# Kernel optimization log

Hardware: AMD Instinct MI355X
Metric: run time of the kernel (lower is better)

## Reference

```python
import jax, jax.numpy as jnp
import numpy as np

B, L, H = 64, 512, 512  # batch_size, input_size (src len), hidden_size


def setup_inputs() -> dict:
    key = jax.random.key(0)
    ks = jax.random.split(key, 12)
    return {
        "encoder_outputs": jax.random.normal(ks[0], (B, L, H), dtype=jnp.float32),
        "attn_mask": jax.random.randint(ks[1], (B, L), 0, 2, dtype=jnp.int64),
        "hidden": jax.random.normal(ks[2], (B, H), dtype=jnp.float32),
        "coverage": jax.random.uniform(ks[3], (B, L), dtype=jnp.float32),
        # attnLin: Linear(H, H)
        "attn_w": jax.random.normal(ks[4], (H, H), dtype=jnp.float32) * 0.02,
        "attn_b": jax.random.normal(ks[5], (H,), dtype=jnp.float32) * 0.02,
        # decoderAttnLinear: Linear(H, H)
        "dec_w": jax.random.normal(ks[6], (H, H), dtype=jnp.float32) * 0.02,
        "dec_b": jax.random.normal(ks[7], (H,), dtype=jnp.float32) * 0.02,
        # cvgConv: Conv2d(L, L, kernel=(1, H), padding='same') -> weight [L, L, 1, H]
        "cvg_w": jax.random.normal(ks[8], (L, L, 1, H), dtype=jnp.float32) * 0.02,
        "cvg_b": jax.random.normal(ks[9], (L,), dtype=jnp.float32) * 0.02,
        # v parameter (trunc_normal in torch; plain normal is fine as a baseline)
        "v": jax.random.normal(ks[10], (B, H), dtype=jnp.float32),
    }


def reference(encoder_outputs, attn_mask, hidden, coverage,
              attn_w, attn_b, dec_w, dec_b, cvg_w, cvg_b, v):
    # Per-position linear loop in torch == one batched linear over [B, L, H].
    enc_feat = jnp.einsum('blh,oh->blo', encoder_outputs, attn_w) + attn_b  # [B,L,H]
    dec_feat = (hidden @ dec_w.T + dec_b)[:, None, :]                        # [B,1,H]
    # Coverage conv: input is [B, L(channels), 1, 1]; kernel (1, H) with 'same'
    # padding means only kernel column kw = (H-1)//2 ever overlaps the single
    # real (non-zero-padded) pixel, so the conv reduces exactly to a matmul
    # with that weight column plus bias. Same math, no wasted zero-multiplies.
    center = (H - 1) // 2
    w_eff = cvg_w[:, :, 0, center]                                           # [L_out, L_in]
    cov_feat = (coverage @ w_eff.T + cvg_b)[:, :, None]                      # [B,L,1]
    feats = jnp.tanh(enc_feat + dec_feat + cov_feat)                         # [B,L,H]
    scores = jnp.einsum('blh,bh->bl', feats, v)                              # [B,L]
    scores = jnp.where(attn_mask == 1, scores, -jnp.inf)
    attn_weights = jax.nn.softmax(scores, axis=1)                            # [B,L]
    new_coverage = coverage + attn_weights                                   # coverage += aw
    context_vector = jnp.einsum('bl,blh->bh', attn_weights, encoder_outputs) # [B,H]
    return context_vector, attn_weights, new_coverage
```

## Files before the change

kernel.cpp:

```cpp
#include <hip/hip_runtime.h>

#define B_ 64
#define L_ 512
#define H_ 512
#define CENTER 255

typedef float  f32x4  __attribute__((ext_vector_type(4)));
typedef _Float16 f16x8 __attribute__((ext_vector_type(8)));
typedef unsigned short u16x4 __attribute__((ext_vector_type(4)));
typedef unsigned short u16x8 __attribute__((ext_vector_type(8)));
typedef unsigned short USH;


__device__ __forceinline__ float fast_tanh(float x) {
    float e = __expf(2.0f * x);
    return 1.0f - 2.0f * __builtin_amdgcn_rcpf(e + 1.0f);
}

__launch_bounds__(512)
__global__ void pre_kernel(const float* __restrict__ cvg_w, const float* __restrict__ cvg_b,
                           const float* __restrict__ coverage,
                           const float* __restrict__ aw, USH* __restrict__ bh16,
                           const float* __restrict__ hidden, const float* __restrict__ dec_w,
                           const float* __restrict__ dec_b,
                           float* __restrict__ dec_feat, float* __restrict__ cov_feat) {
    __shared__ float pool[34304];
    const int bid = blockIdx.x, t = threadIdx.x;
    if (bid < 512) {
        float* wl = pool;
        float* cs = pool + 512;
        const int i = bid;
        wl[t] = cvg_w[((size_t)(i * L_ + t)) * H_ + CENTER];
        #pragma unroll 8
        for (int c = 0; c < 64; ++c)
            cs[t * 65 + c] = coverage[c * L_ + t];
        __syncthreads();
        const int b = t >> 3, jg = t & 7;
        float sum = 0.f;
        #pragma unroll 8
        for (int jj = 0; jj < 64; ++jj) {
            int j = jg * 64 + ((jj + jg * 8) & 63);
            sum += cs[j * 65 + b] * wl[j];
        }
        sum += __shfl_xor(sum, 1, 64);
        sum += __shfl_xor(sum, 2, 64);
        sum += __shfl_xor(sum, 4, 64);
        if (jg == 0) cov_feat[b * L_ + i] = sum + cvg_b[i];
    } else if (bid < 640) {
        int i = (bid - 512) * 512 + t;
        float4 x = *(const float4*)&aw[(size_t)i * 4];
        float xs[4] = {x.x, x.y, x.z, x.w};
        u16x4 h;
        #pragma unroll
        for (int j = 0; j < 4; ++j)
            h[j] = __builtin_bit_cast(USH, (_Float16)xs[j]);
        *(u16x4*)&bh16[(size_t)i * 4] = h;
    } else {
        float* sbuf = pool;
        float* pr   = pool + 512;
        const int blk = bid - 640, b = blk >> 2, qq = blk & 3;
        const int ol = t & 127, part = t >> 7;
        sbuf[t] = hidden[b * H_ + t];
        __syncthreads();
        const float* row  = dec_w + (size_t)(qq * 128 + ol) * H_ + part * 128;
        const float* hseg = sbuf + part * 128;
        float d0 = 0.f, d1 = 0.f, d2 = 0.f, d3 = 0.f;
        #pragma unroll
        for (int k = 0; k < 128; k += 16) {
            float4 w0 = *(const float4*)&row[k];
            float4 w1 = *(const float4*)&row[k + 4];
            float4 w2 = *(const float4*)&row[k + 8];
            float4 w3 = *(const float4*)&row[k + 12];
            d0 += w0.x * hseg[k]      + w0.y * hseg[k + 1]  + w0.z * hseg[k + 2]  + w0.w * hseg[k + 3];
            d1 += w1.x * hseg[k + 4]  + w1.y * hseg[k + 5]  + w1.z * hseg[k + 6]  + w1.w * hseg[k + 7];
            d2 += w2.x * hseg[k + 8]  + w2.y * hseg[k + 9]  + w2.z * hseg[k + 10] + w2.w * hseg[k + 11];
            d3 += w3.x * hseg[k + 12] + w3.y * hseg[k + 13] + w3.z * hseg[k + 14] + w3.w * hseg[k + 15];
        }
        pr[t] = d0 + d1 + d2 + d3;
        __syncthreads();
        if (t < 128)
            dec_feat[b * H_ + qq * 128 + t] = pr[t] + pr[t + 128] + pr[t + 256] + pr[t + 384]
                                              + dec_b[qq * 128 + t];
    }
}

#define BM 128

#define STAGE_B(BUF, KS1)                                                                  \
    {                                                                                      \
        _Pragma("unroll")                                                                  \
        for (int it = 0; it < 2; ++it)                                                     \
            __builtin_amdgcn_global_load_lds(                                              \
                (const __attribute__((address_space(1))) void*)(bh16 + goffB[it] + (KS1) * 32), \
                (__attribute__((address_space(3))) void*)&Bsh[BUF][(wv * 2 + it) * 512],   \
                16, 0, 0);                                                                 \
    }

#define CVTWRITEA2(BUF, A4a, A4b)                                                          \
    {                                                                                      \
        float axs[8] = {A4a.x, A4a.y, A4a.z, A4a.w, A4b.x, A4b.y, A4b.z, A4b.w};           \
        u16x8 hh;                                                                          \
        _Pragma("unroll")                                                                  \
        for (int j = 0; j < 8; ++j)                                                        \
            hh[j] = __builtin_bit_cast(USH, (_Float16)axs[j]);                             \
        *(u16x8*)&Ash[BUF][awoff] = hh;                                                    \
    }

__launch_bounds__(512, 4)
__global__ void fused_score_mfma(const float* __restrict__ enc,
                                 const USH* __restrict__ bh16,
                                 const float* __restrict__ attn_b,
                                 const float* __restrict__ dec_feat,
                                 const float* __restrict__ cov_feat,
                                 const float* __restrict__ v,
                                 float* __restrict__ spart) {
    __shared__ USH Bsh[3][8192];
    __shared__ USH Ash[2][4096];

    const int t  = threadIdx.x;
    const int wv = t >> 6, ln = t & 63;
    const int wr = wv >> 2, wc = wv & 3;
    const int q  = ln >> 4, cl = ln & 15;
    const int mt = blockIdx.x, half = blockIdx.y;
    const int m0 = mt * BM;
    const int b  = mt >> 2;
    const int n0 = half * 256;

    int goffB[2];
    #pragma unroll
    for (int it = 0; it < 2; ++it) {
        int c   = wv * 2 + it;
        int srl = ln >> 3;
        int u   = (ln & 7) ^ (srl & 7);
        int n   = n0 + c * 16 + srl * 2 + (u >> 2);
        goffB[it] = n * 512 + (u & 3) * 8;
    }
    const int sA   = (((cl & 1) * 4 + q) ^ ((cl >> 1) & 7)) * 8;
    const int aoff = wr * 2048 + (cl >> 1) * 64 + sA;
    const int boff = wc * 2048 + (cl >> 1) * 64 + sA;

    const int arow = t >> 2, ak4 = t & 3;
    const int asw  = ((arow & 1) * 4 + ak4) ^ ((arow >> 1) & 7);
    const int awoff = (arow >> 1) * 64 + asw * 8;
    const float* agsrc = enc + (size_t)(m0 + arow) * H_ + ak4 * 8;

    f32x4 acc[4][4];
    #pragma unroll
    for (int mf = 0; mf < 4; ++mf)
        #pragma unroll
        for (int nf = 0; nf < 4; ++nf) acc[mf][nf] = (f32x4){0.f, 0.f, 0.f, 0.f};

    float4 aPa = *(const float4*)(agsrc + 32);
    float4 aPb = *(const float4*)(agsrc + 36);
    float4 c0a = *(const float4*)agsrc;
    float4 c0b = *(const float4*)(agsrc + 4);
    __builtin_amdgcn_sched_barrier(0);
    STAGE_B(0, 0);
    STAGE_B(1, 1);
    __builtin_amdgcn_sched_barrier(0);
    CVTWRITEA2(0, c0a, c0b);
    asm volatile("s_waitcnt lgkmcnt(0)" ::: "memory");
    asm volatile("s_waitcnt vmcnt(2)" ::: "memory");
    __builtin_amdgcn_sched_barrier(0);
    __builtin_amdgcn_s_barrier();

    #pragma unroll
    for (int ks = 0; ks < 16; ++ks) {
        const int curB = ks % 3;
        const int curA = ks & 1, nxtA = curA ^ 1;
        float4 aNa, aNb;
        if (ks < 14) {
            STAGE_B((ks + 2) % 3, ks + 2);
            aNa = *(const float4*)(agsrc + (ks + 2) * 32);
            aNb = *(const float4*)(agsrc + (ks + 2) * 32 + 4);
            __builtin_amdgcn_sched_barrier(0);
        }

        f16x8 ah[4];
        #pragma unroll
        for (int mf = 0; mf < 4; ++mf)
            ah[mf] = *(const f16x8*)&Ash[curA][aoff + mf * 512];
        __builtin_amdgcn_s_setprio(1);
        #pragma unroll
        for (int nf = 0; nf < 4; ++nf) {
            f16x8 bh = *(const f16x8*)&Bsh[curB][boff + nf * 512];
            #pragma unroll
            for (int mf = 0; mf < 4; ++mf)
                acc[mf][nf] = __builtin_amdgcn_mfma_f32_16x16x32_f16(ah[mf], bh, acc[mf][nf], 0, 0, 0);
        }
        __builtin_amdgcn_s_setprio(0);

        if (ks < 15) {
            CVTWRITEA2(nxtA, aPa, aPb);
            aPa = aNa; aPb = aNb;
            asm volatile("s_waitcnt lgkmcnt(0)" ::: "memory");
            if (ks < 14)
                asm volatile("s_waitcnt vmcnt(4)" ::: "memory");
            else
                asm volatile("s_waitcnt vmcnt(0)" ::: "memory");
            __builtin_amdgcn_sched_barrier(0);
            __builtin_amdgcn_s_barrier();
        }
    }
    __syncthreads();

    float (*scred)[BM] = (float (*)[BM])Ash;
    float addv[4], vvv[4];
    #pragma unroll
    for (int nf = 0; nf < 4; ++nf) {
        int n = n0 + wc * 64 + nf * 16 + cl;
        addv[nf] = attn_b[n] + dec_feat[b * H_ + n];
        vvv[nf]  = v[b * H_ + n];
    }
    #pragma unroll
    for (int mf = 0; mf < 4; ++mf) {
        #pragma unroll
        for (int reg = 0; reg < 4; ++reg) {
            int row = wr * 64 + mf * 16 + q * 4 + reg;
            float cf = cov_feat[m0 + row];
            float s = 0.f;
            #pragma unroll
            for (int nf = 0; nf < 4; ++nf)
                s += fast_tanh(acc[mf][nf][reg] + addv[nf] + cf) * vvv[nf];
            s += __shfl_xor(s, 1, 64);
            s += __shfl_xor(s, 2, 64);
            s += __shfl_xor(s, 4, 64);
            s += __shfl_xor(s, 8, 64);
            if (cl == 0) scred[wc][row] = s;
        }
    }
    __syncthreads();
    if (t < BM) {
        float s = 0.f;
        #pragma unroll
        for (int g = 0; g < 4; ++g) s += scred[g][t];
        spart[half * (B_ * L_) + m0 + t] = s;
    }
}

__launch_bounds__(1024)
__global__ void smctx_kernel(const float* __restrict__ spart, const int* __restrict__ mask,
                             const float* __restrict__ coverage, const float* __restrict__ enc,
                             float* __restrict__ out) {
    __shared__ float w[512];
    __shared__ float red[16];
    __shared__ float red2[16];
    __shared__ float4 cred4[32][32];
    const int bid = blockIdx.x, b = bid >> 2, hc = bid & 3, t = threadIdx.x;
    const int wv = t >> 6, ln = t & 63;

    float sv = 0.f; bool mk = false;
    if (t < 512) {
        mk = (mask[b * L_ + t] == 1);
        sv = spart[b * L_ + t] + spart[B_ * L_ + b * L_ + t];
    }
    float val = (t < 512 && mk) ? sv : -INFINITY;

    float r = val;
    #pragma unroll
    for (int d = 1; d <= 32; d <<= 1) r = fmaxf(r, __shfl_xor(r, d, 64));
    if (ln == 0) red[wv] = r;
    __syncthreads();
    float gmax = red[0];
    #pragma unroll
    for (int i = 1; i < 16; ++i) gmax = fmaxf(gmax, red[i]);

    float p = (t < 512 && mk) ? __expf(sv - gmax) : 0.f;
    float qq = p;
    #pragma unroll
    for (int d = 1; d <= 32; d <<= 1) qq += __shfl_xor(qq, d, 64);
    if (ln == 0) red2[wv] = qq;
    __syncthreads();
    float tot = 0.f;
    #pragma unroll
    for (int i = 0; i < 16; ++i) tot += red2[i];

    float wt = p / tot;
    if (t < 512) {
        w[t] = wt;
        if (hc == 0) {
            out[B_ * H_ + b * L_ + t] = wt;
            out[B_ * H_ + B_ * L_ + b * L_ + t] = coverage[b * L_ + t] + wt;
        }
    }
    __syncthreads();

    const int c4 = t & 31, rg = t >> 5;
    const float4* ebase = (const float4*)enc
                          + ((size_t)(b * L_ + rg)) * 128 + hc * 32 + c4;
    float4 a4 = {0.f, 0.f, 0.f, 0.f};
    #pragma unroll
    for (int k = 0; k < 16; ++k) {
        float wl_ = w[rg + 32 * k];
        float4 e = ebase[(size_t)(32 * k) * 128];
        a4.x += wl_ * e.x; a4.y += wl_ * e.y; a4.z += wl_ * e.z; a4.w += wl_ * e.w;
    }
    cred4[rg][c4] = a4;
    __syncthreads();
    if (t < 32) {
        float4 s = {0.f, 0.f, 0.f, 0.f};
        #pragma unroll
        for (int g = 0; g < 32; ++g) {
            float4 c = cred4[g][t];
            s.x += c.x; s.y += c.y; s.z += c.z; s.w += c.w;
        }
        *(float4*)&out[b * H_ + hc * 128 + t * 4] = s;
    }
}

extern "C" void kernel_launch(void* const* d_in, const int* in_sizes, int n_in,
                              void* d_out, int out_size, void* d_ws, size_t ws_size,
                              hipStream_t stream) {
    const float* enc      = (const float*)d_in[0];
    const int*   mask     = (const int*)d_in[1];
    const float* hidden   = (const float*)d_in[2];
    const float* coverage = (const float*)d_in[3];
    const float* attn_w   = (const float*)d_in[4];
    const float* attn_b   = (const float*)d_in[5];
    const float* dec_w    = (const float*)d_in[6];
    const float* dec_b    = (const float*)d_in[7];
    const float* cvg_w    = (const float*)d_in[8];
    const float* cvg_b    = (const float*)d_in[9];
    const float* v        = (const float*)d_in[10];
    float* out = (float*)d_out;
    float* ws  = (float*)d_ws;
    float* dec_feat = ws + 32768;
    float* cov_feat = ws + 65536;
    float* spart    = ws + 98304;
    USH* bpk = (USH*)(ws + 360448);

    hipLaunchKernelGGL(pre_kernel,       dim3(896),     dim3(512),  0, stream,
                       cvg_w, cvg_b, coverage, attn_w, bpk, hidden, dec_w, dec_b,
                       dec_feat, cov_feat);
    hipLaunchKernelGGL(fused_score_mfma, dim3(256, 2),  dim3(512),  0, stream,
                       enc, bpk, attn_b, dec_feat, cov_feat, v, spart);
    hipLaunchKernelGGL(smctx_kernel,     dim3(256),     dim3(1024), 0, stream,
                       spart, mask, coverage, enc, out);
}
```

Baseline: 67.43 us.

## Merge pre_kernel's three block roles into uniform 256-block launch

Replaces the heterogeneous 896-block pre_kernel (separate blocks for coverage conv, weight fp16 conversion, and decoder linear) with 256 uniform blocks that each do all three jobs: two coverage-conv outputs, a slice of the weight conversion, and a quarter-row of the decoder linear. The coverage tile load is shared across two output columns and the wave-count imbalance between block types is removed. In exchange, each block uses more LDS (about 136 KB for the full cs array plus buffers), which limits occupancy, and the kernel runs fewer, longer blocks.

```diff
diff --git a/kernel.cpp b/kernel.cpp
--- a/kernel.cpp
+++ b/kernel.cpp
@@ -24,30 +24,18 @@
                            const float* __restrict__ hidden, const float* __restrict__ dec_w,
                            const float* __restrict__ dec_b,
                            float* __restrict__ dec_feat, float* __restrict__ cov_feat) {
-    __shared__ float pool[34304];
+    __shared__ float wl2[1024];
+    __shared__ float cs[512 * 65];
+    __shared__ float sbuf[512];
+    __shared__ float pr[512];
     const int bid = blockIdx.x, t = threadIdx.x;
-    if (bid < 512) {
-        float* wl = pool;
-        float* cs = pool + 512;
-        const int i = bid;
-        wl[t] = cvg_w[((size_t)(i * L_ + t)) * H_ + CENTER];
-        #pragma unroll 8
-        for (int c = 0; c < 64; ++c)
-            cs[t * 65 + c] = coverage[c * L_ + t];
-        __syncthreads();
-        const int b = t >> 3, jg = t & 7;
-        float sum = 0.f;
-        #pragma unroll 8
-        for (int jj = 0; jj < 64; ++jj) {
-            int j = jg * 64 + ((jj + jg * 8) & 63);
-            sum += cs[j * 65 + b] * wl[j];
-        }
-        sum += __shfl_xor(sum, 1, 64);
-        sum += __shfl_xor(sum, 2, 64);
-        sum += __shfl_xor(sum, 4, 64);
-        if (jg == 0) cov_feat[b * L_ + i] = sum + cvg_b[i];
-    } else if (bid < 640) {
-        int i = (bid - 512) * 512 + t;
+    const int i0 = bid, i1 = bid + 256;
+
+    wl2[t]       = cvg_w[((size_t)(i0 * L_ + t)) * H_ + CENTER];
+    wl2[512 + t] = cvg_w[((size_t)(i1 * L_ + t)) * H_ + CENTER];
+
+    if (t < 256) {
+        int i = bid * 256 + t;
         float4 x = *(const float4*)&aw[(size_t)i * 4];
         float xs[4] = {x.x, x.y, x.z, x.w};
         u16x4 h;
@@ -55,13 +43,14 @@
         for (int j = 0; j < 4; ++j)
             h[j] = __builtin_bit_cast(USH, (_Float16)xs[j]);
         *(u16x4*)&bh16[(size_t)i * 4] = h;
-    } else {
-        float* sbuf = pool;
-        float* pr   = pool + 512;
-        const int blk = bid - 640, b = blk >> 2, qq = blk & 3;
-        const int ol = t & 127, part = t >> 7;
-        sbuf[t] = hidden[b * H_ + t];
-        __syncthreads();
+    }
+
+    const int b = bid >> 2, qq = bid & 3;
+    const int ol = t & 127, part = t >> 7;
+    sbuf[t] = hidden[b * H_ + t];
+    __syncthreads();
+
+    {
         const float* row  = dec_w + (size_t)(qq * 128 + ol) * H_ + part * 128;
         const float* hseg = sbuf + part * 128;
         float d0 = 0.f, d1 = 0.f, d2 = 0.f, d3 = 0.f;
@@ -77,10 +66,37 @@
             d3 += w3.x * hseg[k + 12] + w3.y * hseg[k + 13] + w3.z * hseg[k + 14] + w3.w * hseg[k + 15];
         }
         pr[t] = d0 + d1 + d2 + d3;
-        __syncthreads();
-        if (t < 128)
-            dec_feat[b * H_ + qq * 128 + t] = pr[t] + pr[t + 128] + pr[t + 256] + pr[t + 384]
-                                              + dec_b[qq * 128 + t];
+    }
+
+    #pragma unroll 8
+    for (int c = 0; c < 64; ++c)
+        cs[t * 65 + c] = coverage[c * L_ + t];
+    __syncthreads();
+
+    if (t < 128)
+        dec_feat[b * H_ + qq * 128 + t] = pr[t] + pr[t + 128] + pr[t + 256] + pr[t + 384]
+                                          + dec_b[qq * 128 + t];
+
+    {
+        const int bb = t >> 3, jg = t & 7;
+        float s0 = 0.f, s1 = 0.f;
+        #pragma unroll 8
+        for (int jj = 0; jj < 64; ++jj) {
+            int j = jg * 64 + ((jj + jg * 8) & 63);
+            float c = cs[j * 65 + bb];
+            s0 += c * wl2[j];
+            s1 += c * wl2[512 + j];
+        }
+        s0 += __shfl_xor(s0, 1, 64);
+        s0 += __shfl_xor(s0, 2, 64);
+        s0 += __shfl_xor(s0, 4, 64);
+        s1 += __shfl_xor(s1, 1, 64);
+        s1 += __shfl_xor(s1, 2, 64);
+        s1 += __shfl_xor(s1, 4, 64);
+        if (jg == 0) {
+            cov_feat[bb * L_ + i0] = s0 + cvg_b[i0];
+            cov_feat[bb * L_ + i1] = s1 + cvg_b[i1];
+        }
     }
 }
 
@@ -329,7 +345,7 @@
     float* spart    = ws + 98304;
     USH* bpk = (USH*)(ws + 360448);
 
-    hipLaunchKernelGGL(pre_kernel,       dim3(896),     dim3(512),  0, stream,
+    hipLaunchKernelGGL(pre_kernel,       dim3(256),     dim3(512),  0, stream,
                        cvg_w, cvg_b, coverage, attn_w, bpk, hidden, dec_w, dec_b,
                        dec_feat, cov_feat);
     hipLaunchKernelGGL(fused_score_mfma, dim3(256, 2),  dim3(512),  0, stream,
```

After: 64.70 us. 4.1% less time.
